# Optimization experiments

Hardware: AMD Instinct MI355X
Metric: run time of the kernel (lower is better)

The kernel has to match this reference:

```python
import jax, jax.numpy as jnp
import numpy as np

TAU = 1.0
NUM_NEURONS = 32768
INPUT_SIZE = 8192
BATCH = 512


def setup_inputs() -> dict:
    key = jax.random.key(0)
    k1, k2, k3 = jax.random.split(key, 3)
    x = jax.random.uniform(k1, (BATCH, INPUT_SIZE), dtype=jnp.float32)
    gate_weights = jax.random.normal(k2, (NUM_NEURONS, 16), dtype=jnp.float32)
    input_idx = jax.random.randint(k3, (NUM_NEURONS, 2), 0, INPUT_SIZE, dtype=jnp.int32)
    return {"x": x, "gate_weights": gate_weights, "input_idx": input_idx}


def _all_logic_ops(a, b):
    # 16 soft (real-valued) binary logic gates, stacked on last axis.
    ab = a * b
    one = jnp.ones_like(a)
    zero = jnp.zeros_like(a)
    return jnp.stack([
        zero,                  # FALSE
        ab,                    # a AND b
        a - ab,                # a AND NOT b
        a,                     # a
        b - ab,                # NOT a AND b
        b,                     # b
        a + b - 2.0 * ab,      # a XOR b
        a + b - ab,            # a OR b
        1.0 - (a + b - ab),    # NOR
        1.0 - (a + b - 2.0 * ab),  # XNOR
        1.0 - b,               # NOT b
        1.0 - b + ab,          # a OR NOT b
        1.0 - a,               # NOT a
        1.0 - a + ab,          # NOT a OR b
        1.0 - ab,              # NAND
        one,                   # TRUE
    ], axis=-1)  # (B, N, 16)


def reference(x, gate_weights, input_idx):
    # gather the two input columns per neuron: (B, N)
    a = x[:, input_idx[:, 0]]
    b = x[:, input_idx[:, 1]]
    ops = _all_logic_ops(a, b)                          # (B, N, 16)
    w = jax.nn.softmax(gate_weights / TAU, axis=1)      # (N, 16)
    out = jnp.einsum('bnk,nk->bn', ops, w)              # (B, N)
    return out
```

## Files before the change

### kernel.cpp

```cpp
#include <hip/hip_runtime.h>
#include <hip/hip_bf16.h>

#define NUM_NEURONS 32768
#define INPUT_SIZE  8192
#define BATCH       512

typedef float f32x4 __attribute__((ext_vector_type(4)));

__global__ __launch_bounds__(256) void logic_coeff_kernel(
    const float* __restrict__ gw, float4* __restrict__ coeffs)
{
    const int n = blockIdx.x * 256 + threadIdx.x;
    if (n >= NUM_NEURONS) return;
    const float* g = gw + (size_t)n * 16;

    float w[16];
#pragma unroll
    for (int i = 0; i < 16; i += 4) {
        float4 v = *reinterpret_cast<const float4*>(g + i);
        w[i+0] = v.x; w[i+1] = v.y; w[i+2] = v.z; w[i+3] = v.w;
    }
    float m = w[0];
#pragma unroll
    for (int i = 1; i < 16; ++i) m = fmaxf(m, w[i]);
    float s = 0.f;
#pragma unroll
    for (int i = 0; i < 16; ++i) { w[i] = expf(w[i] - m); s += w[i]; }
    const float inv = 1.0f / s;

    const float C0  = (w[8] + w[9] + w[10] + w[11] + w[12] + w[13] + w[14] + w[15]) * inv;
    const float Ca  = (w[2] + w[3] + w[6] + w[7] - w[8] - w[9] - w[12] - w[13]) * inv;
    const float Cb  = (w[4] + w[5] + w[6] + w[7] - w[8] - w[9] - w[10] - w[11]) * inv;
    const float Cab = (w[1] - w[2] - w[4] - 2.f*w[6] - w[7]
                       + w[8] + 2.f*w[9] + w[11] + w[13] - w[14]) * inv;

    coeffs[n] = make_float4(C0, Ca, Cb, Cab);
}

constexpr int CHUNK  = 2048;
constexpr int NPT    = CHUNK / 256;
constexpr int NGRP   = NPT / 4;
constexpr int ROWS_PER_BLOCK = 8;
constexpr int XF4    = INPUT_SIZE / 4 / 256;
constexpr int NCHUNKS = NUM_NEURONS / CHUNK;
constexpr int NROWG   = BATCH / ROWS_PER_BLOCK;
constexpr int NXCD    = 8;

__global__ __launch_bounds__(256, 4) void logic_main_kernel(
    const float*  __restrict__ x,
    const float4* __restrict__ coeffs,
    const int4*   __restrict__ idx4,
    float*        __restrict__ out)
{
    __shared__ float sx[INPUT_SIZE];

    const int tid = threadIdx.x;

    const int bid    = blockIdx.x;
    const int xcd    = bid % NXCD;
    const int within = bid / NXCD;
    const int chunkI = within % NCHUNKS;
    const int rowgI  = xcd * (NROWG / NXCD) + within / NCHUNKS;
    const int chunk0 = chunkI * CHUNK;
    const int row0   = rowgI * ROWS_PER_BLOCK;

    float4 c[NPT];
    int2   id[NPT];
#pragma unroll
    for (int g = 0; g < NGRP; ++g) {
        const int nbase = chunk0 + g * 1024 + tid * 4;
#pragma unroll
        for (int j = 0; j < 4; ++j) c[g*4+j] = coeffs[nbase + j];
        const int4 p0 = idx4[(nbase >> 1) + 0];
        const int4 p1 = idx4[(nbase >> 1) + 1];
        id[g*4+0] = make_int2(p0.x, p0.y);
        id[g*4+1] = make_int2(p0.z, p0.w);
        id[g*4+2] = make_int2(p1.x, p1.y);
        id[g*4+3] = make_int2(p1.z, p1.w);
    }

    float4* s4 = reinterpret_cast<float4*>(sx);

    for (int r = 0; r < ROWS_PER_BLOCK; ++r) {
        const int row = row0 + r;
        if (r) __syncthreads();

        const float4* xrow = reinterpret_cast<const float4*>(x + (size_t)row * INPUT_SIZE);
#pragma unroll
        for (int i = 0; i < XF4; ++i) {
            __builtin_amdgcn_global_load_lds(
                (const __attribute__((address_space(1))) void*)(xrow + i * 256 + tid),
                (__attribute__((address_space(3))) void*)(s4 + i * 256 + tid),
                16, 0, 0);
        }
        __syncthreads();

        f32x4* o = reinterpret_cast<f32x4*>(out + (size_t)row * NUM_NEURONS + chunk0) ;
#pragma unroll
        for (int g = 0; g < NGRP; ++g) {
            f32x4 res;
#pragma unroll
            for (int j = 0; j < 4; ++j) {
                const float4 cc = c[g*4+j];
                const float a = sx[id[g*4+j].x];
                const float b = sx[id[g*4+j].y];
                res[j] = fmaf(a, fmaf(cc.w, b, cc.y), fmaf(cc.z, b, cc.x));
            }
            __builtin_nontemporal_store(res, o + g * 256 + tid);
        }
    }
}

extern "C" void kernel_launch(void* const* d_in, const int* in_sizes, int n_in,
                              void* d_out, int out_size, void* d_ws, size_t ws_size,
                              hipStream_t stream)
{
    const float* x   = (const float*)d_in[0];
    const float* gw  = (const float*)d_in[1];
    const int4*  idx = (const int4*)d_in[2];
    float* out = (float*)d_out;

    float4* coeffs = (float4*)d_ws;

    logic_coeff_kernel<<<NUM_NEURONS / 256, 256, 0, stream>>>(gw, coeffs);

    const int nblocks = NCHUNKS * NROWG;
    logic_main_kernel<<<nblocks, 256, 0, stream>>>(x, coeffs, idx, out);
}
```

Before: 109.8 us.

## Fuse softmax coefficient computation into main kernel and double-buffer x rows in LDS

Removes the separate coefficient kernel: each block now computes the softmax-derived gate coefficients for its neuron chunk directly from gate_weights, using __expf without max subtraction, while the first x row is loading. The single LDS row buffer becomes a double buffer, so the next row's global-to-LDS load overlaps computation on the current row, with manual vmcnt waits and barriers. This saves a kernel launch and the coefficient round trip through memory, and hides row-load latency. In exchange, gate_weights are re-read and the softmax is recomputed by every row group, LDS use doubles (which lowers occupancy), and softmax without max subtraction can overflow for large weights.

```diff
diff --git a/kernel.cpp b/kernel.cpp
--- a/kernel.cpp
+++ b/kernel.cpp
@@ -7,85 +7,36 @@
 
 typedef float f32x4 __attribute__((ext_vector_type(4)));
 
-__global__ __launch_bounds__(256) void logic_coeff_kernel(
-    const float* __restrict__ gw, float4* __restrict__ coeffs)
-{
-    const int n = blockIdx.x * 256 + threadIdx.x;
-    if (n >= NUM_NEURONS) return;
-    const float* g = gw + (size_t)n * 16;
-
-    float w[16];
-#pragma unroll
-    for (int i = 0; i < 16; i += 4) {
-        float4 v = *reinterpret_cast<const float4*>(g + i);
-        w[i+0] = v.x; w[i+1] = v.y; w[i+2] = v.z; w[i+3] = v.w;
-    }
-    float m = w[0];
-#pragma unroll
-    for (int i = 1; i < 16; ++i) m = fmaxf(m, w[i]);
-    float s = 0.f;
-#pragma unroll
-    for (int i = 0; i < 16; ++i) { w[i] = expf(w[i] - m); s += w[i]; }
-    const float inv = 1.0f / s;
-
-    const float C0  = (w[8] + w[9] + w[10] + w[11] + w[12] + w[13] + w[14] + w[15]) * inv;
-    const float Ca  = (w[2] + w[3] + w[6] + w[7] - w[8] - w[9] - w[12] - w[13]) * inv;
-    const float Cb  = (w[4] + w[5] + w[6] + w[7] - w[8] - w[9] - w[10] - w[11]) * inv;
-    const float Cab = (w[1] - w[2] - w[4] - 2.f*w[6] - w[7]
-                       + w[8] + 2.f*w[9] + w[11] + w[13] - w[14]) * inv;
-
-    coeffs[n] = make_float4(C0, Ca, Cb, Cab);
-}
-
 constexpr int CHUNK  = 2048;
 constexpr int NPT    = CHUNK / 256;
 constexpr int NGRP   = NPT / 4;
-constexpr int ROWS_PER_BLOCK = 8;
+constexpr int RPB    = 8;
 constexpr int XF4    = INPUT_SIZE / 4 / 256;
 constexpr int NCHUNKS = NUM_NEURONS / CHUNK;
-constexpr int NROWG   = BATCH / ROWS_PER_BLOCK;
+constexpr int NROWG   = BATCH / RPB;
 constexpr int NXCD    = 8;
 
-__global__ __launch_bounds__(256, 4) void logic_main_kernel(
-    const float*  __restrict__ x,
-    const float4* __restrict__ coeffs,
-    const int4*   __restrict__ idx4,
-    float*        __restrict__ out)
+__global__ __launch_bounds__(256) void logic_main_kernel(
+    const float* __restrict__ x,
+    const float* __restrict__ gw,
+    const int4*  __restrict__ idx4,
+    float*       __restrict__ out)
 {
-    __shared__ float sx[INPUT_SIZE];
+    __shared__ float sx[2][INPUT_SIZE];
 
     const int tid = threadIdx.x;
 
     const int bid    = blockIdx.x;
-    const int xcd    = bid % NXCD;
-    const int within = bid / NXCD;
-    const int chunkI = within % NCHUNKS;
-    const int rowgI  = xcd * (NROWG / NXCD) + within / NCHUNKS;
+    const int xcd    = bid & (NXCD - 1);
+    const int within = bid >> 3;
+    const int chunkI = within & (NCHUNKS - 1);
+    const int rowgI  = xcd * (NROWG / NXCD) + (within >> 4);
     const int chunk0 = chunkI * CHUNK;
-    const int row0   = rowgI * ROWS_PER_BLOCK;
+    const int row0   = rowgI * RPB;
 
-    float4 c[NPT];
-    int2   id[NPT];
-#pragma unroll
-    for (int g = 0; g < NGRP; ++g) {
-        const int nbase = chunk0 + g * 1024 + tid * 4;
-#pragma unroll
-        for (int j = 0; j < 4; ++j) c[g*4+j] = coeffs[nbase + j];
-        const int4 p0 = idx4[(nbase >> 1) + 0];
-        const int4 p1 = idx4[(nbase >> 1) + 1];
-        id[g*4+0] = make_int2(p0.x, p0.y);
-        id[g*4+1] = make_int2(p0.z, p0.w);
-        id[g*4+2] = make_int2(p1.x, p1.y);
-        id[g*4+3] = make_int2(p1.z, p1.w);
-    }
-
-    float4* s4 = reinterpret_cast<float4*>(sx);
-
-    for (int r = 0; r < ROWS_PER_BLOCK; ++r) {
-        const int row = row0 + r;
-        if (r) __syncthreads();
-
+    auto stage = [&](int buf, int row) {
         const float4* xrow = reinterpret_cast<const float4*>(x + (size_t)row * INPUT_SIZE);
+        float4* s4 = reinterpret_cast<float4*>(sx[buf]);
 #pragma unroll
         for (int i = 0; i < XF4; ++i) {
             __builtin_amdgcn_global_load_lds(
@@ -93,20 +44,69 @@
                 (__attribute__((address_space(3))) void*)(s4 + i * 256 + tid),
                 16, 0, 0);
         }
-        __syncthreads();
+    };
+    stage(0, row0);
 
-        f32x4* o = reinterpret_cast<f32x4*>(out + (size_t)row * NUM_NEURONS + chunk0) ;
+    float4 c[NPT];
+    int2   id[NPT];
+#pragma unroll
+    for (int g = 0; g < NGRP; ++g) {
+        const int nbase = chunk0 + g * 1024 + tid * 4;
+        const int4 p0 = idx4[(nbase >> 1) + 0];
+        const int4 p1 = idx4[(nbase >> 1) + 1];
+        id[g*4+0] = make_int2(p0.x, p0.y);
+        id[g*4+1] = make_int2(p0.z, p0.w);
+        id[g*4+2] = make_int2(p1.x, p1.y);
+        id[g*4+3] = make_int2(p1.z, p1.w);
+#pragma unroll
+        for (int j = 0; j < 4; ++j) {
+            const float* gg = gw + (size_t)(nbase + j) * 16;
+            float w[16];
+#pragma unroll
+            for (int i = 0; i < 16; i += 4) {
+                float4 v = *reinterpret_cast<const float4*>(gg + i);
+                w[i+0] = v.x; w[i+1] = v.y; w[i+2] = v.z; w[i+3] = v.w;
+            }
+            float s = 0.f;
+#pragma unroll
+            for (int i = 0; i < 16; ++i) { w[i] = __expf(w[i]); s += w[i]; }
+            const float inv = 1.0f / s;
+            const float C0  = (w[8] + w[9] + w[10] + w[11] + w[12] + w[13] + w[14] + w[15]) * inv;
+            const float Ca  = (w[2] + w[3] + w[6] + w[7] - w[8] - w[9] - w[12] - w[13]) * inv;
+            const float Cb  = (w[4] + w[5] + w[6] + w[7] - w[8] - w[9] - w[10] - w[11]) * inv;
+            const float Cab = (w[1] - w[2] - w[4] - 2.f*w[6] - w[7]
+                               + w[8] + 2.f*w[9] + w[11] + w[13] - w[14]) * inv;
+            c[g*4+j] = make_float4(C0, Ca, Cb, Cab);
+        }
+    }
+
+    asm volatile("s_waitcnt vmcnt(0)" ::: "memory");
+    __builtin_amdgcn_s_barrier();
+
+#pragma unroll
+    for (int r = 0; r < RPB; ++r) {
+        const int cur = r & 1;
+        if (r + 1 < RPB) stage(cur ^ 1, row0 + r + 1);
+        asm volatile("" ::: "memory");
+
+        const int row = row0 + r;
+        f32x4* o = reinterpret_cast<f32x4*>(out + (size_t)row * NUM_NEURONS + chunk0);
 #pragma unroll
         for (int g = 0; g < NGRP; ++g) {
             f32x4 res;
 #pragma unroll
             for (int j = 0; j < 4; ++j) {
                 const float4 cc = c[g*4+j];
-                const float a = sx[id[g*4+j].x];
-                const float b = sx[id[g*4+j].y];
+                const float a = sx[cur][id[g*4+j].x];
+                const float b = sx[cur][id[g*4+j].y];
                 res[j] = fmaf(a, fmaf(cc.w, b, cc.y), fmaf(cc.z, b, cc.x));
             }
             __builtin_nontemporal_store(res, o + g * 256 + tid);
+        }
+
+        if (r + 1 < RPB) {
+            asm volatile("s_waitcnt vmcnt(2)" ::: "memory");
+            __builtin_amdgcn_s_barrier();
         }
     }
 }
@@ -120,10 +120,6 @@
     const int4*  idx = (const int4*)d_in[2];
     float* out = (float*)d_out;
 
-    float4* coeffs = (float4*)d_ws;
-
-    logic_coeff_kernel<<<NUM_NEURONS / 256, 256, 0, stream>>>(gw, coeffs);
-
     const int nblocks = NCHUNKS * NROWG;
-    logic_main_kernel<<<nblocks, 256, 0, stream>>>(x, coeffs, idx, out);
+    logic_main_kernel<<<nblocks, 256, 0, stream>>>(x, gw, idx, out);
 }
```

Result: slower. 115.8 us (+5.4%).
